# Performance work log

Measured on AMD Instinct MI355X. Metric: run time of the kernel, lower is better.

## Reference

```python
import jax, jax.numpy as jnp
import numpy as np

DIM = 192
HEADS = 6
WIN = (2, 7, 7)
N = WIN[0] * WIN[1] * WIN[2]  # 98
B_ = 2048
NW = 512


def _relative_position_index():
    d, h, w = np.meshgrid(np.arange(WIN[0]), np.arange(WIN[1]), np.arange(WIN[2]), indexing='ij')
    coords = np.stack([d.ravel(), h.ravel(), w.ravel()])  # [3, N]
    rel = coords[:, :, None] - coords[:, None, :]          # [3, N, N]
    rel = rel.transpose(1, 2, 0).astype(np.int64)
    rel[:, :, 0] += WIN[0] - 1
    rel[:, :, 1] += WIN[1] - 1
    rel[:, :, 2] += WIN[2] - 1
    rel[:, :, 0] *= (2 * WIN[1] - 1) * (2 * WIN[2] - 1)
    rel[:, :, 1] *= 2 * WIN[2] - 1
    return rel.sum(-1).astype(np.int32)  # [N, N]


def setup_inputs() -> dict:
    key = jax.random.key(0)
    ks = jax.random.split(key, 6)
    table_size = (2 * WIN[0] - 1) * (2 * WIN[1] - 1) * (2 * WIN[2] - 1)  # 507
    return {
        'x': jax.random.normal(ks[0], (B_, N, DIM), dtype=jnp.float32),
        'mask': jnp.zeros((NW, N, N), dtype=jnp.float32),
        'qkv_w': jax.random.normal(ks[1], (3 * DIM, DIM), dtype=jnp.float32) * 0.02,
        'qkv_b': jnp.zeros((3 * DIM,), dtype=jnp.float32),
        'proj_w': jax.random.normal(ks[2], (DIM, DIM), dtype=jnp.float32) * 0.02,
        'proj_b': jnp.zeros((DIM,), dtype=jnp.float32),
        'bias_table': jax.random.truncated_normal(ks[3], -2.0, 2.0, (table_size, HEADS), dtype=jnp.float32) * 0.02,
        'rel_idx': jnp.asarray(_relative_position_index()),
    }


def reference(x, mask, qkv_w, qkv_b, proj_w, proj_b, bias_table, rel_idx):
    b_, n, c = x.shape
    hd = c // HEADS
    scale = hd ** -0.5
    qkv = x @ qkv_w.T + qkv_b                      # [B_, N, 3C]
    qkv = qkv.reshape(b_, n, 3, HEADS, hd).transpose(2, 0, 3, 1, 4)
    q, k, v = qkv[0], qkv[1], qkv[2]               # each [B_, H, N, hd]
    attn = jnp.einsum('bhnd,bhmd->bhnm', q * scale, k)
    # relative position bias gather: [N*N] -> [N, N, H] -> [H, N, N]
    bias = bias_table[rel_idx.reshape(-1)].reshape(n, n, HEADS).transpose(2, 0, 1)
    attn = attn + bias[None]
    nw = mask.shape[0]
    attn = attn.reshape(b_ // nw, nw, HEADS, n, n) + mask[None, :, None]
    attn = attn.reshape(b_, HEADS, n, n)
    attn = jax.nn.softmax(attn, axis=-1)
    out = jnp.einsum('bhnm,bhmd->bhnd', attn, v)   # [B_, H, N, hd]
    out = out.transpose(0, 2, 1, 3).reshape(b_, n, c)
    return out @ proj_w.T + proj_b
```

## Files before the change

### kernel.cpp

```cpp
#include <hip/hip_runtime.h>
#include <hip/hip_bf16.h>
#include <stdint.h>

#define SEQ    98
#define DIMC   192
#define NHEADS 6
#define HDIM   32
#define NBATCH 2048
#define NWIN   512
#define SCALE  0.17677669529663687f

#define OFF_QKVW  0u
#define OFF_PROJW 221184u
#define OFF_BIAS  294912u
#define OFF_FLAGS 445440u
#define OFF_Q     447488u
#define PERWIN_E  18816
#define PERWIN_B  ((size_t)PERWIN_E * 2 * 4)

typedef __attribute__((ext_vector_type(4)))  float f32x4;
typedef __attribute__((ext_vector_type(8)))  short bf16x8;

static __device__ __forceinline__ uint16_t f2bf(float f) {
    uint32_t u = __builtin_bit_cast(uint32_t, f);
    u += 0x7fffu + ((u >> 16) & 1u);
    return (uint16_t)(u >> 16);
}
static __device__ __forceinline__ float bf2f(uint16_t h) {
    uint32_t u = ((uint32_t)h) << 16;
    return __builtin_bit_cast(float, u);
}
static __device__ __forceinline__ uint32_t cvtpk(float a, float b) {
    uint32_t d;
    asm("v_cvt_pk_bf16_f32 %0, %1, %2" : "=v"(d) : "v"(a), "v"(b));
    return d;
}

__global__ void __launch_bounds__(256) k_prep(
    const float* __restrict__ qkv_w, const float* __restrict__ proj_w,
    const float* __restrict__ bias_table, const int* __restrict__ rel_idx,
    uint16_t* __restrict__ qkv_wb, uint16_t* __restrict__ proj_wb,
    uint16_t* __restrict__ bias6b)
{
    int idx = blockIdx.x * 256 + threadIdx.x;
    if (idx < 110592) {
        qkv_wb[idx] = f2bf(qkv_w[idx]);
    } else if (idx < 147456) {
        int t = idx - 110592;
        proj_wb[t] = f2bf(proj_w[t]);
    } else {
        int t = idx - 147456;
        int h = t / (112 * 112);
        int rr = t % (112 * 112);
        int i = rr / 112, j = rr % 112;
        float v = -1e30f;
        if (i < SEQ && j < SEQ) v = bias_table[rel_idx[i * SEQ + j] * NHEADS + h];
        bias6b[t] = f2bf(v);
    }
}

__global__ void __launch_bounds__(256) k_flags(const float* __restrict__ mask,
                                               int* __restrict__ flags)
{
    int w = blockIdx.x;
    __shared__ int sf;
    if (threadIdx.x == 0) sf = 0;
    __syncthreads();
    const float* m = mask + (size_t)w * (SEQ * SEQ);
    int local = 0;
    for (int i = threadIdx.x; i < SEQ * SEQ; i += 256) local |= (m[i] != 0.0f);
    if (local) atomicOr(&sf, 1);
    __syncthreads();
    if (threadIdx.x == 0) flags[w] = sf;
}

__global__ void __launch_bounds__(256, 4) k_qkv(
    const float* __restrict__ x, const float* __restrict__ qkv_b,
    const uint16_t* __restrict__ qkv_wb,
    uint16_t* __restrict__ q_ws, uint16_t* __restrict__ k_ws,
    uint16_t* __restrict__ v_ws, int b0)
{
    __shared__ uint16_t xs[112][200];
    __shared__ uint16_t obuf[4][16][40];
    const int lb = blockIdx.x, b = b0 + lb, tid = threadIdx.x;
    const int lane = tid & 63, wave = tid >> 6;
    const int l15 = lane & 15, lq = lane >> 4;

    const float4* x4 = (const float4*)(x + (size_t)b * SEQ * DIMC);
    for (int i = tid; i < SEQ * DIMC / 4; i += 256) {
        float4 v = x4[i];
        int row = i / 48, col = (i % 48) * 4;
        uint2 pk;
        pk.x = cvtpk(v.x, v.y);
        pk.y = cvtpk(v.z, v.w);
        *(uint2*)&xs[row][col] = pk;
    }
    __syncthreads();

    for (int ot = wave; ot < 18; ot += 4) {
        bf16x8 bfr[2][6];
        float qb[2];
        #pragma unroll
        for (int o = 0; o < 2; o++) {
            const uint16_t* wp = qkv_wb + (size_t)(ot * 32 + o * 16 + l15) * DIMC + lq * 8;
            #pragma unroll
            for (int kk = 0; kk < 6; kk++) bfr[o][kk] = *(const bf16x8*)(wp + kk * 32);
            qb[o] = qkv_b[ot * 32 + o * 16 + l15];
        }
        const int sec = ot / 6, head = ot % 6;
        uint16_t* outp = (sec == 0 ? q_ws : sec == 1 ? k_ws : v_ws)
                       + (size_t)(lb * NHEADS + head) * (SEQ * HDIM);
        for (int mt = 0; mt < 7; mt++) {
            bf16x8 afr[6];
            #pragma unroll
            for (int kk = 0; kk < 6; kk++)
                afr[kk] = *(const bf16x8*)&xs[mt * 16 + l15][kk * 32 + lq * 8];
            f32x4 a0 = {0.f,0.f,0.f,0.f}, a1 = {0.f,0.f,0.f,0.f};
            #pragma unroll
            for (int kk = 0; kk < 6; kk++) {
                a0 = __builtin_amdgcn_mfma_f32_16x16x32_bf16(afr[kk], bfr[0][kk], a0, 0, 0, 0);
                a1 = __builtin_amdgcn_mfma_f32_16x16x32_bf16(afr[kk], bfr[1][kk], a1, 0, 0, 0);
            }
            #pragma unroll
            for (int r = 0; r < 4; r++) {
                obuf[wave][lq * 4 + r][l15]      = f2bf(a0[r] + qb[0]);
                obuf[wave][lq * 4 + r][16 + l15] = f2bf(a1[r] + qb[1]);
            }
            int r16 = lane >> 2, m8 = (lane & 3) * 8;
            int token = mt * 16 + r16;
            bf16x8 ov = *(const bf16x8*)&obuf[wave][r16][m8];
            if (token < SEQ)
                *(bf16x8*)(outp + token * HDIM + m8) = ov;
        }
    }
}

__global__ void __launch_bounds__(256, 4) k_attn(
    const uint16_t* __restrict__ q_ws, const uint16_t* __restrict__ k_ws,
    const uint16_t* __restrict__ v_ws, const uint16_t* __restrict__ bias6b,
    const float* __restrict__ mask, const int* __restrict__ flags,
    uint16_t* __restrict__ att, int b0)
{
    __shared__ uint16_t k_s[98][40];
    __shared__ uint16_t vT_s[32][136];
    __shared__ uint16_t ps[4][16][40];

    const int bid = blockIdx.x;
    const int lb = bid / 6, h = bid % 6;
    const int bg = b0 + lb;
    const int tid = threadIdx.x, lane = tid & 63, wave = tid >> 6;
    const int l15 = lane & 15, lq = lane >> 4;
    const int useMask = flags[bg & (NWIN - 1)];
    const float* maskp = mask + (size_t)(bg & (NWIN - 1)) * (SEQ * SEQ);

    for (int i = tid; i < 32 * 19; i += 256) {
        int d = i / 19, c = 98 + (i % 19) * 2;
        *(uint32_t*)&vT_s[d][c] = 0;
    }
    const uint32_t* kp = (const uint32_t*)(k_ws + (size_t)(lb * NHEADS + h) * (SEQ * HDIM));
    const uint32_t* vp = (const uint32_t*)(v_ws + (size_t)(lb * NHEADS + h) * (SEQ * HDIM));
    for (int i = tid; i < SEQ * 16; i += 256) {
        int row = i >> 4, cp = i & 15;
        uint32_t kv = kp[i];
        *(uint32_t*)&k_s[row][cp * 2] = kv;
        uint32_t vv = vp[i];
        vT_s[cp * 2][row]     = (uint16_t)(vv & 0xffff);
        vT_s[cp * 2 + 1][row] = (uint16_t)(vv >> 16);
    }
    __syncthreads();

    const uint16_t* qbase = q_ws + (size_t)(lb * NHEADS + h) * (SEQ * HDIM);
    for (int mt = wave; mt < 7; mt += 4) {
        int qrow = mt * 16 + l15; if (qrow > 97) qrow = 97;
        bf16x8 aq = *(const bf16x8*)(qbase + qrow * HDIM + lq * 8);

        float p[7][4], rowmax[4], rowsum[4];
        #pragma unroll
        for (int r = 0; r < 4; r++) rowmax[r] = -3e38f;
        #pragma unroll
        for (int jt = 0; jt < 7; jt++) {
            int krow = jt * 16 + l15; if (krow > 97) krow = 97;
            bf16x8 bk = *(const bf16x8*)&k_s[krow][lq * 8];
            f32x4 z = {0.f,0.f,0.f,0.f};
            f32x4 s4 = __builtin_amdgcn_mfma_f32_16x16x32_bf16(aq, bk, z, 0, 0, 0);
            int j = jt * 16 + l15;
            #pragma unroll
            for (int r = 0; r < 4; r++) {
                int i_ = mt * 16 + lq * 4 + r;
                float s = s4[r] * SCALE + bf2f(bias6b[(h * 112 + i_) * 112 + j]);
                if (useMask && i_ < SEQ && j < SEQ) s += maskp[i_ * SEQ + j];
                p[jt][r] = s;
                rowmax[r] = fmaxf(rowmax[r], s);
            }
        }
        #pragma unroll
        for (int r = 0; r < 4; r++) {
            float m = rowmax[r];
            m = fmaxf(m, __shfl_xor(m, 1));
            m = fmaxf(m, __shfl_xor(m, 2));
            m = fmaxf(m, __shfl_xor(m, 4));
            m = fmaxf(m, __shfl_xor(m, 8));
            rowmax[r] = m; rowsum[r] = 0.f;
        }
        #pragma unroll
        for (int jt = 0; jt < 7; jt++)
            #pragma unroll
            for (int r = 0; r < 4; r++) {
                float e = __expf(p[jt][r] - rowmax[r]);
                p[jt][r] = e; rowsum[r] += e;
            }
        #pragma unroll
        for (int r = 0; r < 4; r++) {
            float s2 = rowsum[r];
            s2 += __shfl_xor(s2, 1); s2 += __shfl_xor(s2, 2);
            s2 += __shfl_xor(s2, 4); s2 += __shfl_xor(s2, 8);
            rowsum[r] = 1.0f / s2;
        }

        f32x4 o0 = {0.f,0.f,0.f,0.f}, o1 = {0.f,0.f,0.f,0.f};
        #pragma unroll
        for (int kk = 0; kk < 4; kk++) {
            #pragma unroll
            for (int r = 0; r < 4; r++) {
                ps[wave][lq * 4 + r][l15]      = f2bf(p[2 * kk][r]);
                ps[wave][lq * 4 + r][16 + l15] = f2bf(2 * kk + 1 < 7 ? p[2 * kk + 1][r] : 0.f);
            }
            bf16x8 ap  = *(const bf16x8*)&ps[wave][l15][lq * 8];
            bf16x8 bv0 = *(const bf16x8*)&vT_s[l15][kk * 32 + lq * 8];
            bf16x8 bv1 = *(const bf16x8*)&vT_s[16 + l15][kk * 32 + lq * 8];
            o0 = __builtin_amdgcn_mfma_f32_16x16x32_bf16(ap, bv0, o0, 0, 0, 0);
            o1 = __builtin_amdgcn_mfma_f32_16x16x32_bf16(ap, bv1, o1, 0, 0, 0);
        }
        #pragma unroll
        for (int r = 0; r < 4; r++) {
            ps[wave][lq * 4 + r][l15]      = f2bf(o0[r] * rowsum[r]);
            ps[wave][lq * 4 + r][16 + l15] = f2bf(o1[r] * rowsum[r]);
        }
        int r16 = lane >> 2, m8 = (lane & 3) * 8;
        int token = mt * 16 + r16;
        bf16x8 ov = *(const bf16x8*)&ps[wave][r16][m8];
        if (token < SEQ)
            *(bf16x8*)(att + ((size_t)lb * SEQ + token) * DIMC + h * HDIM + m8) = ov;
    }
}

__global__ void __launch_bounds__(256, 4) k_proj(
    const uint16_t* __restrict__ att, const uint16_t* __restrict__ proj_wb,
    const float* __restrict__ proj_b, float* __restrict__ out, int M)
{
    __shared__ uint16_t as_[64][200];
    const int blk = blockIdx.x, tid = threadIdx.x;
    const int lane = tid & 63, wave = tid >> 6;
    const int l15 = lane & 15, lq = lane >> 4;

    for (int i = tid; i < 64 * DIMC / 8; i += 256) {
        int el = i * 8;
        int lr = el / DIMC, c = el % DIMC;
        int gr = blk * 64 + lr; if (gr >= M) gr = M - 1;
        *(bf16x8*)&as_[lr][c] = *(const bf16x8*)(att + (size_t)gr * DIMC + c);
    }
    __syncthreads();

    bf16x8 a[6];
    #pragma unroll
    for (int kk = 0; kk < 6; kk++)
        a[kk] = *(const bf16x8*)&as_[wave * 16 + l15][kk * 32 + lq * 8];

    for (int ot = 0; ot < 12; ot++) {
        const uint16_t* wp = proj_wb + (size_t)(ot * 16 + l15) * DIMC + lq * 8;
        f32x4 acc = {0.f,0.f,0.f,0.f};
        #pragma unroll
        for (int kk = 0; kk < 6; kk++) {
            bf16x8 bw = *(const bf16x8*)(wp + kk * 32);
            acc = __builtin_amdgcn_mfma_f32_16x16x32_bf16(a[kk], bw, acc, 0, 0, 0);
        }
        float pb = proj_b[ot * 16 + l15];
        #pragma unroll
        for (int r = 0; r < 4; r++) {
            int gr = blk * 64 + wave * 16 + lq * 4 + r;
            if (gr < M) out[(size_t)gr * DIMC + ot * 16 + l15] = acc[r] + pb;
        }
    }
}

extern "C" void kernel_launch(void* const* d_in, const int* in_sizes, int n_in,
                              void* d_out, int out_size, void* d_ws, size_t ws_size,
                              hipStream_t stream) {
    const float* x          = (const float*)d_in[0];
    const float* mask       = (const float*)d_in[1];
    const float* qkv_w      = (const float*)d_in[2];
    const float* qkv_b      = (const float*)d_in[3];
    const float* proj_w     = (const float*)d_in[4];
    const float* proj_b     = (const float*)d_in[5];
    const float* bias_table = (const float*)d_in[6];
    const int*   rel_idx    = (const int*)d_in[7];
    float* out = (float*)d_out;
    char*  ws  = (char*)d_ws;

    uint16_t* qkv_wb  = (uint16_t*)(ws + OFF_QKVW);
    uint16_t* proj_wb = (uint16_t*)(ws + OFF_PROJW);
    uint16_t* bias6b  = (uint16_t*)(ws + OFF_BIAS);
    int*      flags   = (int*)(ws + OFF_FLAGS);

    int chunk = NBATCH;
    if (ws_size < (size_t)OFF_Q + (size_t)NBATCH * PERWIN_B) {
        size_t cap = ws_size > OFF_Q ? (ws_size - OFF_Q) / PERWIN_B : 1;
        if (cap < 1) cap = 1;
        if (cap > NBATCH) cap = NBATCH;
        chunk = (int)cap;
    }
    uint16_t* q_ws   = (uint16_t*)(ws + OFF_Q);
    uint16_t* k_ws   = q_ws + (size_t)chunk * PERWIN_E;
    uint16_t* v_ws   = k_ws + (size_t)chunk * PERWIN_E;
    uint16_t* att_ws = v_ws + (size_t)chunk * PERWIN_E;

    k_prep<<<870, 256, 0, stream>>>(qkv_w, proj_w, bias_table, rel_idx,
                                    qkv_wb, proj_wb, bias6b);
    k_flags<<<NWIN, 256, 0, stream>>>(mask, flags);
    for (int b0 = 0; b0 < NBATCH; b0 += chunk) {
        int nb = chunk < NBATCH - b0 ? chunk : NBATCH - b0;
        k_qkv<<<nb, 256, 0, stream>>>(x, qkv_b, qkv_wb, q_ws, k_ws, v_ws, b0);
        k_attn<<<nb * NHEADS, 256, 0, stream>>>(q_ws, k_ws, v_ws, bias6b, mask,
                                                flags, att_ws, b0);
        int M = nb * SEQ;
        k_proj<<<(M + 63) / 64, 256, 0, stream>>>(att_ws, proj_wb, proj_b,
                                                  out + (size_t)b0 * SEQ * DIMC, M);
    }
}
```

Measured before the change: 716.2 us.

## Fuse QKV projection, windowed attention and output projection into one kernel per window

Replaces the three kernels (qkv, attention, proj) and their bf16 global workspace round-trips with one 512-thread kernel per window. Q, K, transposed V and the attention output stay in LDS. Heads are processed in two groups of three to bound LDS use. This removes the global writes and reads of the intermediate q/k/v/att tensors and two launches. In exchange it uses a large LDS footprint (about 130KB), which limits occupancy to about one block per CU, and QKV weights are reloaded per block.

```diff
diff --git a/kernel.cpp b/kernel.cpp
--- a/kernel.cpp
+++ b/kernel.cpp
@@ -14,9 +14,6 @@
 #define OFF_PROJW 221184u
 #define OFF_BIAS  294912u
 #define OFF_FLAGS 445440u
-#define OFF_Q     447488u
-#define PERWIN_E  18816
-#define PERWIN_B  ((size_t)PERWIN_E * 2 * 4)
 
 typedef __attribute__((ext_vector_type(4)))  float f32x4;
 typedef __attribute__((ext_vector_type(8)))  short bf16x8;
@@ -74,20 +71,33 @@
     if (threadIdx.x == 0) flags[w] = sf;
 }
 
-__global__ void __launch_bounds__(256, 4) k_qkv(
+__global__ void __launch_bounds__(512, 2) k_fused(
     const float* __restrict__ x, const float* __restrict__ qkv_b,
-    const uint16_t* __restrict__ qkv_wb,
-    uint16_t* __restrict__ q_ws, uint16_t* __restrict__ k_ws,
-    uint16_t* __restrict__ v_ws, int b0)
+    const uint16_t* __restrict__ qkv_wb, const uint16_t* __restrict__ bias6b,
+    const float* __restrict__ mask, const int* __restrict__ flags,
+    const uint16_t* __restrict__ proj_wb, const float* __restrict__ proj_b,
+    float* __restrict__ out)
 {
-    __shared__ uint16_t xs[112][200];
-    __shared__ uint16_t obuf[4][16][40];
-    const int lb = blockIdx.x, b = b0 + lb, tid = threadIdx.x;
+    __shared__ uint16_t xs[98][200];
+    __shared__ uint16_t q_s[3][98][40];
+    __shared__ uint16_t k_s[3][98][40];
+    __shared__ uint16_t vT_s[3][32][136];
+    __shared__ uint16_t att_s[98][200];
+    __shared__ uint16_t ps[8][16][40];
+
+    const int b = blockIdx.x, tid = threadIdx.x;
     const int lane = tid & 63, wave = tid >> 6;
     const int l15 = lane & 15, lq = lane >> 4;
-
+    const int wdx = b & (NWIN - 1);
+    const int useMask = flags[wdx];
+    const float* maskp = mask + (size_t)wdx * (SEQ * SEQ);
+
+    for (int i = tid; i < 3 * 32 * 19; i += 512) {
+        int hd = i / 19, c = 98 + (i % 19) * 2;
+        *(uint32_t*)&vT_s[hd >> 5][hd & 31][c] = 0;
+    }
     const float4* x4 = (const float4*)(x + (size_t)b * SEQ * DIMC);
-    for (int i = tid; i < SEQ * DIMC / 4; i += 256) {
+    for (int i = tid; i < SEQ * DIMC / 4; i += 512) {
         float4 v = x4[i];
         int row = i / 48, col = (i % 48) * 4;
         uint2 pk;
@@ -97,188 +107,141 @@
     }
     __syncthreads();
 
-    for (int ot = wave; ot < 18; ot += 4) {
-        bf16x8 bfr[2][6];
-        float qb[2];
+    for (int g = 0; g < 2; g++) {
+        if (g) __syncthreads();
+
+        for (int u = wave; u < 36; u += 8) {
+            int ot = u >> 1, half = u & 1;
+            int sec = ot / 6, rem = ot % 6, hl = rem >> 1, dh = rem & 1;
+            int wrow = sec * 192 + (3 * g + hl) * 32 + dh * 16 + l15;
+            const uint16_t* wp = qkv_wb + (size_t)wrow * DIMC + lq * 8;
+            bf16x8 bfr[6];
+            #pragma unroll
+            for (int kk = 0; kk < 6; kk++) bfr[kk] = *(const bf16x8*)(wp + kk * 32);
+            float qb = qkv_b[wrow];
+            int mt0 = half ? 4 : 0, mt1 = half ? 7 : 4;
+            for (int mt = mt0; mt < mt1; mt++) {
+                int ar = mt * 16 + l15; if (ar > 97) ar = 97;
+                bf16x8 afr[6];
+                #pragma unroll
+                for (int kk = 0; kk < 6; kk++)
+                    afr[kk] = *(const bf16x8*)&xs[ar][kk * 32 + lq * 8];
+                f32x4 acc = {0.f, 0.f, 0.f, 0.f};
+                #pragma unroll
+                for (int kk = 0; kk < 6; kk++)
+                    acc = __builtin_amdgcn_mfma_f32_16x16x32_bf16(afr[kk], bfr[kk], acc, 0, 0, 0);
+                #pragma unroll
+                for (int r = 0; r < 4; r++) {
+                    int row = mt * 16 + lq * 4 + r;
+                    if (row < SEQ) {
+                        uint16_t vv = f2bf(acc[r] + qb);
+                        if (sec == 0)      q_s[hl][row][dh * 16 + l15] = vv;
+                        else if (sec == 1) k_s[hl][row][dh * 16 + l15] = vv;
+                        else               vT_s[hl][dh * 16 + l15][row] = vv;
+                    }
+                }
+            }
+        }
+        __syncthreads();
+
+        for (int t = wave; t < 21; t += 8) {
+            int hl = t / 7, mt = t % 7, H = 3 * g + hl;
+            int qrow = mt * 16 + l15; if (qrow > 97) qrow = 97;
+            bf16x8 aq = *(const bf16x8*)&q_s[hl][qrow][lq * 8];
+
+            float p[7][4], rowmax[4], rowsum[4];
+            #pragma unroll
+            for (int r = 0; r < 4; r++) rowmax[r] = -3e38f;
+            #pragma unroll
+            for (int jt = 0; jt < 7; jt++) {
+                int krow = jt * 16 + l15; if (krow > 97) krow = 97;
+                bf16x8 bk = *(const bf16x8*)&k_s[hl][krow][lq * 8];
+                f32x4 z = {0.f, 0.f, 0.f, 0.f};
+                f32x4 s4 = __builtin_amdgcn_mfma_f32_16x16x32_bf16(aq, bk, z, 0, 0, 0);
+                int j = jt * 16 + l15;
+                #pragma unroll
+                for (int r = 0; r < 4; r++) {
+                    int i_ = mt * 16 + lq * 4 + r;
+                    float s = s4[r] * SCALE + bf2f(bias6b[(H * 112 + i_) * 112 + j]);
+                    if (useMask && i_ < SEQ && j < SEQ) s += maskp[i_ * SEQ + j];
+                    p[jt][r] = s;
+                    rowmax[r] = fmaxf(rowmax[r], s);
+                }
+            }
+            #pragma unroll
+            for (int r = 0; r < 4; r++) {
+                float m = rowmax[r];
+                m = fmaxf(m, __shfl_xor(m, 1));
+                m = fmaxf(m, __shfl_xor(m, 2));
+                m = fmaxf(m, __shfl_xor(m, 4));
+                m = fmaxf(m, __shfl_xor(m, 8));
+                rowmax[r] = m; rowsum[r] = 0.f;
+            }
+            #pragma unroll
+            for (int jt = 0; jt < 7; jt++)
+                #pragma unroll
+                for (int r = 0; r < 4; r++) {
+                    float e = __expf(p[jt][r] - rowmax[r]);
+                    p[jt][r] = e; rowsum[r] += e;
+                }
+            #pragma unroll
+            for (int r = 0; r < 4; r++) {
+                float s2 = rowsum[r];
+                s2 += __shfl_xor(s2, 1); s2 += __shfl_xor(s2, 2);
+                s2 += __shfl_xor(s2, 4); s2 += __shfl_xor(s2, 8);
+                rowsum[r] = 1.0f / s2;
+            }
+
+            f32x4 o0 = {0.f,0.f,0.f,0.f}, o1 = {0.f,0.f,0.f,0.f};
+            #pragma unroll
+            for (int kk = 0; kk < 4; kk++) {
+                #pragma unroll
+                for (int r = 0; r < 4; r++) {
+                    ps[wave][lq * 4 + r][l15]      = f2bf(p[2 * kk][r]);
+                    ps[wave][lq * 4 + r][16 + l15] = f2bf(2 * kk + 1 < 7 ? p[2 * kk + 1][r] : 0.f);
+                }
+                bf16x8 ap  = *(const bf16x8*)&ps[wave][l15][lq * 8];
+                bf16x8 bv0 = *(const bf16x8*)&vT_s[hl][l15][kk * 32 + lq * 8];
+                bf16x8 bv1 = *(const bf16x8*)&vT_s[hl][16 + l15][kk * 32 + lq * 8];
+                o0 = __builtin_amdgcn_mfma_f32_16x16x32_bf16(ap, bv0, o0, 0, 0, 0);
+                o1 = __builtin_amdgcn_mfma_f32_16x16x32_bf16(ap, bv1, o1, 0, 0, 0);
+            }
+            #pragma unroll
+            for (int r = 0; r < 4; r++) {
+                int row = mt * 16 + lq * 4 + r;
+                if (row < SEQ) {
+                    att_s[row][H * HDIM + l15]      = f2bf(o0[r] * rowsum[r]);
+                    att_s[row][H * HDIM + 16 + l15] = f2bf(o1[r] * rowsum[r]);
+                }
+            }
+        }
+    }
+    __syncthreads();
+
+    for (int u = wave; u < 24; u += 8) {
+        int ot = u >> 1, half = u & 1;
+        const uint16_t* wp = proj_wb + (size_t)(ot * 16 + l15) * DIMC + lq * 8;
+        bf16x8 bw[6];
         #pragma unroll
-        for (int o = 0; o < 2; o++) {
-            const uint16_t* wp = qkv_wb + (size_t)(ot * 32 + o * 16 + l15) * DIMC + lq * 8;
-            #pragma unroll
-            for (int kk = 0; kk < 6; kk++) bfr[o][kk] = *(const bf16x8*)(wp + kk * 32);
-            qb[o] = qkv_b[ot * 32 + o * 16 + l15];
-        }
-        const int sec = ot / 6, head = ot % 6;
-        uint16_t* outp = (sec == 0 ? q_ws : sec == 1 ? k_ws : v_ws)
-                       + (size_t)(lb * NHEADS + head) * (SEQ * HDIM);
-        for (int mt = 0; mt < 7; mt++) {
-            bf16x8 afr[6];
+        for (int kk = 0; kk < 6; kk++) bw[kk] = *(const bf16x8*)(wp + kk * 32);
+        float pb = proj_b[ot * 16 + l15];
+        int mt0 = half ? 4 : 0, mt1 = half ? 7 : 4;
+        for (int mt = mt0; mt < mt1; mt++) {
+            int arow = mt * 16 + l15; if (arow > 97) arow = 97;
+            bf16x8 aa[6];
             #pragma unroll
             for (int kk = 0; kk < 6; kk++)
-                afr[kk] = *(const bf16x8*)&xs[mt * 16 + l15][kk * 32 + lq * 8];
-            f32x4 a0 = {0.f,0.f,0.f,0.f}, a1 = {0.f,0.f,0.f,0.f};
-            #pragma unroll
-            for (int kk = 0; kk < 6; kk++) {
-                a0 = __builtin_amdgcn_mfma_f32_16x16x32_bf16(afr[kk], bfr[0][kk], a0, 0, 0, 0);
-                a1 = __builtin_amdgcn_mfma_f32_16x16x32_bf16(afr[kk], bfr[1][kk], a1, 0, 0, 0);
-            }
-            #pragma unroll
-            for (int r = 0; r < 4; r++) {
-                obuf[wave][lq * 4 + r][l15]      = f2bf(a0[r] + qb[0]);
-                obuf[wave][lq * 4 + r][16 + l15] = f2bf(a1[r] + qb[1]);
-            }
-            int r16 = lane >> 2, m8 = (lane & 3) * 8;
-            int token = mt * 16 + r16;
-            bf16x8 ov = *(const bf16x8*)&obuf[wave][r16][m8];
-            if (token < SEQ)
-                *(bf16x8*)(outp + token * HDIM + m8) = ov;
-        }
-    }
-}
-
-__global__ void __launch_bounds__(256, 4) k_attn(
-    const uint16_t* __restrict__ q_ws, const uint16_t* __restrict__ k_ws,
-    const uint16_t* __restrict__ v_ws, const uint16_t* __restrict__ bias6b,
-    const float* __restrict__ mask, const int* __restrict__ flags,
-    uint16_t* __restrict__ att, int b0)
-{
-    __shared__ uint16_t k_s[98][40];
-    __shared__ uint16_t vT_s[32][136];
-    __shared__ uint16_t ps[4][16][40];
-
-    const int bid = blockIdx.x;
-    const int lb = bid / 6, h = bid % 6;
-    const int bg = b0 + lb;
-    const int tid = threadIdx.x, lane = tid & 63, wave = tid >> 6;
-    const int l15 = lane & 15, lq = lane >> 4;
-    const int useMask = flags[bg & (NWIN - 1)];
-    const float* maskp = mask + (size_t)(bg & (NWIN - 1)) * (SEQ * SEQ);
-
-    for (int i = tid; i < 32 * 19; i += 256) {
-        int d = i / 19, c = 98 + (i % 19) * 2;
-        *(uint32_t*)&vT_s[d][c] = 0;
-    }
-    const uint32_t* kp = (const uint32_t*)(k_ws + (size_t)(lb * NHEADS + h) * (SEQ * HDIM));
-    const uint32_t* vp = (const uint32_t*)(v_ws + (size_t)(lb * NHEADS + h) * (SEQ * HDIM));
-    for (int i = tid; i < SEQ * 16; i += 256) {
-        int row = i >> 4, cp = i & 15;
-        uint32_t kv = kp[i];
-        *(uint32_t*)&k_s[row][cp * 2] = kv;
-        uint32_t vv = vp[i];
-        vT_s[cp * 2][row]     = (uint16_t)(vv & 0xffff);
-        vT_s[cp * 2 + 1][row] = (uint16_t)(vv >> 16);
-    }
-    __syncthreads();
-
-    const uint16_t* qbase = q_ws + (size_t)(lb * NHEADS + h) * (SEQ * HDIM);
-    for (int mt = wave; mt < 7; mt += 4) {
-        int qrow = mt * 16 + l15; if (qrow > 97) qrow = 97;
-        bf16x8 aq = *(const bf16x8*)(qbase + qrow * HDIM + lq * 8);
-
-        float p[7][4], rowmax[4], rowsum[4];
-        #pragma unroll
-        for (int r = 0; r < 4; r++) rowmax[r] = -3e38f;
-        #pragma unroll
-        for (int jt = 0; jt < 7; jt++) {
-            int krow = jt * 16 + l15; if (krow > 97) krow = 97;
-            bf16x8 bk = *(const bf16x8*)&k_s[krow][lq * 8];
-            f32x4 z = {0.f,0.f,0.f,0.f};
-            f32x4 s4 = __builtin_amdgcn_mfma_f32_16x16x32_bf16(aq, bk, z, 0, 0, 0);
-            int j = jt * 16 + l15;
-            #pragma unroll
-            for (int r = 0; r < 4; r++) {
-                int i_ = mt * 16 + lq * 4 + r;
-                float s = s4[r] * SCALE + bf2f(bias6b[(h * 112 + i_) * 112 + j]);
-                if (useMask && i_ < SEQ && j < SEQ) s += maskp[i_ * SEQ + j];
-                p[jt][r] = s;
-                rowmax[r] = fmaxf(rowmax[r], s);
-            }
-        }
-        #pragma unroll
-        for (int r = 0; r < 4; r++) {
-            float m = rowmax[r];
-            m = fmaxf(m, __shfl_xor(m, 1));
-            m = fmaxf(m, __shfl_xor(m, 2));
-            m = fmaxf(m, __shfl_xor(m, 4));
-            m = fmaxf(m, __shfl_xor(m, 8));
-            rowmax[r] = m; rowsum[r] = 0.f;
-        }
-        #pragma unroll
-        for (int jt = 0; jt < 7; jt++)
-            #pragma unroll
-            for (int r = 0; r < 4; r++) {
-                float e = __expf(p[jt][r] - rowmax[r]);
-                p[jt][r] = e; rowsum[r] += e;
-            }
-        #pragma unroll
-        for (int r = 0; r < 4; r++) {
-            float s2 = rowsum[r];
-            s2 += __shfl_xor(s2, 1); s2 += __shfl_xor(s2, 2);
-            s2 += __shfl_xor(s2, 4); s2 += __shfl_xor(s2, 8);
-            rowsum[r] = 1.0f / s2;
-        }
-
-        f32x4 o0 = {0.f,0.f,0.f,0.f}, o1 = {0.f,0.f,0.f,0.f};
-        #pragma unroll
-        for (int kk = 0; kk < 4; kk++) {
-            #pragma unroll
-            for (int r = 0; r < 4; r++) {
-                ps[wave][lq * 4 + r][l15]      = f2bf(p[2 * kk][r]);
-                ps[wave][lq * 4 + r][16 + l15] = f2bf(2 * kk + 1 < 7 ? p[2 * kk + 1][r] : 0.f);
-            }
-            bf16x8 ap  = *(const bf16x8*)&ps[wave][l15][lq * 8];
-            bf16x8 bv0 = *(const bf16x8*)&vT_s[l15][kk * 32 + lq * 8];
-            bf16x8 bv1 = *(const bf16x8*)&vT_s[16 + l15][kk * 32 + lq * 8];
-            o0 = __builtin_amdgcn_mfma_f32_16x16x32_bf16(ap, bv0, o0, 0, 0, 0);
-            o1 = __builtin_amdgcn_mfma_f32_16x16x32_bf16(ap, bv1, o1, 0, 0, 0);
-        }
-        #pragma unroll
-        for (int r = 0; r < 4; r++) {
-            ps[wave][lq * 4 + r][l15]      = f2bf(o0[r] * rowsum[r]);
-            ps[wave][lq * 4 + r][16 + l15] = f2bf(o1[r] * rowsum[r]);
-        }
-        int r16 = lane >> 2, m8 = (lane & 3) * 8;
-        int token = mt * 16 + r16;
-        bf16x8 ov = *(const bf16x8*)&ps[wave][r16][m8];
-        if (token < SEQ)
-            *(bf16x8*)(att + ((size_t)lb * SEQ + token) * DIMC + h * HDIM + m8) = ov;
-    }
-}
-
-__global__ void __launch_bounds__(256, 4) k_proj(
-    const uint16_t* __restrict__ att, const uint16_t* __restrict__ proj_wb,
-    const float* __restrict__ proj_b, float* __restrict__ out, int M)
-{
-    __shared__ uint16_t as_[64][200];
-    const int blk = blockIdx.x, tid = threadIdx.x;
-    const int lane = tid & 63, wave = tid >> 6;
-    const int l15 = lane & 15, lq = lane >> 4;
-
-    for (int i = tid; i < 64 * DIMC / 8; i += 256) {
-        int el = i * 8;
-        int lr = el / DIMC, c = el % DIMC;
-        int gr = blk * 64 + lr; if (gr >= M) gr = M - 1;
-        *(bf16x8*)&as_[lr][c] = *(const bf16x8*)(att + (size_t)gr * DIMC + c);
-    }
-    __syncthreads();
-
-    bf16x8 a[6];
-    #pragma unroll
-    for (int kk = 0; kk < 6; kk++)
-        a[kk] = *(const bf16x8*)&as_[wave * 16 + l15][kk * 32 + lq * 8];
-
-    for (int ot = 0; ot < 12; ot++) {
-        const uint16_t* wp = proj_wb + (size_t)(ot * 16 + l15) * DIMC + lq * 8;
-        f32x4 acc = {0.f,0.f,0.f,0.f};
-        #pragma unroll
-        for (int kk = 0; kk < 6; kk++) {
-            bf16x8 bw = *(const bf16x8*)(wp + kk * 32);
-            acc = __builtin_amdgcn_mfma_f32_16x16x32_bf16(a[kk], bw, acc, 0, 0, 0);
-        }
-        float pb = proj_b[ot * 16 + l15];
-        #pragma unroll
-        for (int r = 0; r < 4; r++) {
-            int gr = blk * 64 + wave * 16 + lq * 4 + r;
-            if (gr < M) out[(size_t)gr * DIMC + ot * 16 + l15] = acc[r] + pb;
+                aa[kk] = *(const bf16x8*)&att_s[arow][kk * 32 + lq * 8];
+            f32x4 acc = {0.f, 0.f, 0.f, 0.f};
+            #pragma unroll
+            for (int kk = 0; kk < 6; kk++)
+                acc = __builtin_amdgcn_mfma_f32_16x16x32_bf16(aa[kk], bw[kk], acc, 0, 0, 0);
+            #pragma unroll
+            for (int r = 0; r < 4; r++) {
+                int row = mt * 16 + lq * 4 + r;
+                if (row < SEQ)
+                    out[((size_t)b * SEQ + row) * DIMC + ot * 16 + l15] = acc[r] + pb;
+            }
         }
     }
 }
@@ -302,28 +265,9 @@
     uint16_t* bias6b  = (uint16_t*)(ws + OFF_BIAS);
     int*      flags   = (int*)(ws + OFF_FLAGS);
 
-    int chunk = NBATCH;
-    if (ws_size < (size_t)OFF_Q + (size_t)NBATCH * PERWIN_B) {
-        size_t cap = ws_size > OFF_Q ? (ws_size - OFF_Q) / PERWIN_B : 1;
-        if (cap < 1) cap = 1;
-        if (cap > NBATCH) cap = NBATCH;
-        chunk = (int)cap;
-    }
-    uint16_t* q_ws   = (uint16_t*)(ws + OFF_Q);
-    uint16_t* k_ws   = q_ws + (size_t)chunk * PERWIN_E;
-    uint16_t* v_ws   = k_ws + (size_t)chunk * PERWIN_E;
-    uint16_t* att_ws = v_ws + (size_t)chunk * PERWIN_E;
-
     k_prep<<<870, 256, 0, stream>>>(qkv_w, proj_w, bias_table, rel_idx,
                                     qkv_wb, proj_wb, bias6b);
     k_flags<<<NWIN, 256, 0, stream>>>(mask, flags);
-    for (int b0 = 0; b0 < NBATCH; b0 += chunk) {
-        int nb = chunk < NBATCH - b0 ? chunk : NBATCH - b0;
-        k_qkv<<<nb, 256, 0, stream>>>(x, qkv_b, qkv_wb, q_ws, k_ws, v_ws, b0);
-        k_attn<<<nb * NHEADS, 256, 0, stream>>>(q_ws, k_ws, v_ws, bias6b, mask,
-                                                flags, att_ws, b0);
-        int M = nb * SEQ;
-        k_proj<<<(M + 63) / 64, 256, 0, stream>>>(att_ws, proj_wb, proj_b,
-                                                  out + (size_t)b0 * SEQ * DIMC, M);
-    }
-}
+    k_fused<<<NBATCH, 512, 0, stream>>>(x, qkv_b, qkv_wb, bias6b, mask, flags,
+                                        proj_wb, proj_b, out);
+}
```

Measured after the change: 741.2 us. +3.5%, slower.
